# Kernel optimization log

Hardware: AMD Instinct MI355X
Metric: run time of the kernel (lower is better)

## Reference

```python
import jax, jax.numpy as jnp
import numpy as np

B, T, H, OUT = 16384, 128, 256, 10
EPS = 1e-5


def setup_inputs() -> dict:
    key = jax.random.key(0)
    ks = jax.random.split(key, 8)
    x = jax.random.randint(ks[0], (B, T, 1), 0, 10).astype(jnp.float32)
    def lin(k, fan_out, fan_in):
        bound = 1.0 / np.sqrt(fan_in)
        kw, kb = jax.random.split(k)
        w = jax.random.uniform(kw, (fan_out, fan_in), jnp.float32, -bound, bound)
        b = jax.random.uniform(kb, (fan_out,), jnp.float32, -bound, bound)
        return w, b
    embed_w, embed_b = lin(ks[1], H, 1)
    update_w, update_b = lin(ks[2], H, H)
    out_w, out_b = lin(ks[3], OUT, H)
    return {
        "x": x,
        "embed_w": embed_w, "embed_b": embed_b,
        "update_w": update_w, "update_b": update_b,
        "gamma": jnp.ones((H,), jnp.float32), "beta": jnp.zeros((H,), jnp.float32),
        "out_w": out_w, "out_b": out_b,
    }


def _layer_norm(h, gamma, beta):
    mu = jnp.mean(h, axis=-1, keepdims=True)
    var = jnp.mean(jnp.square(h - mu), axis=-1, keepdims=True)
    return (h - mu) * jax.lax.rsqrt(var + EPS) * gamma + beta


def reference(x, embed_w, embed_b, update_w, update_b, gamma, beta, out_w, out_b):
    # embed is per-timestep independent -> precompute for all T at once: [B,T,H]
    inp_all = jnp.tanh(jnp.einsum('bti,hi->bth', x, embed_w) + embed_b)

    def step(h, inp_t):  # h:[B,H], inp_t:[B,H]
        h = jnp.tanh((inp_t + h) @ update_w.T + update_b)
        h = _layer_norm(h, gamma, beta)
        return h, None

    h0 = jnp.zeros((x.shape[0], embed_w.shape[0]), x.dtype)
    h, _ = jax.lax.scan(step, h0, jnp.swapaxes(inp_all, 0, 1))  # scan over T
    return h @ out_w.T + out_b  # [B, 10]
```

## Files before the change

kernel.cpp:

```cpp
#include <hip/hip_runtime.h>
#include <hip/hip_fp16.h>
#include <math.h>

typedef _Float16 f16;
typedef _Float16 f16x8 __attribute__((ext_vector_type(8)));
typedef float f32x4 __attribute__((ext_vector_type(4)));
typedef unsigned char u8;

#define HDIM 256
#define TST 128
#define OUTD 10
#define S2LE 2.8853900817779268f

__global__ __launch_bounds__(256, 2) void rnn_kernel(
    const float* __restrict__ x,
    const float* __restrict__ embed_w,
    const float* __restrict__ embed_b,
    const float* __restrict__ update_w,
    const float* __restrict__ update_b,
    const float* __restrict__ gamma,
    const float* __restrict__ beta,
    const float* __restrict__ out_w,
    const float* __restrict__ out_b,
    float* __restrict__ out)
{
  __shared__ __align__(16) f16   sFR[2][2][8][64][8];
  __shared__ __align__(16) float sD1[10 * 260];
  __shared__ __align__(16) float sBW[HDIM];
  __shared__ __align__(16) float sRSg[HDIM];
  __shared__ __align__(16) float sST[2][32][12];
  __shared__ float sOB[16];
  __shared__ u8    sXb[TST][32];

  const int tid = threadIdx.x;
  const int w  = tid >> 6;
  const int l  = tid & 63;
  const int q  = l >> 4;
  const int ml = l & 15;
  const int base = blockIdx.x * 32;
  const int nb = w * 64 + q * 4;

  float* T0 = (float*)&sFR[0][0][0][0][0];

  {
    float ew = embed_w[tid], eb = embed_b[tid];
    #pragma unroll
    for (int xv = 0; xv < 10; xv++)
      T0[tid * 10 + xv] = tanhf((float)xv * ew + eb);
  }
  for (int idx = tid; idx < 32 * TST; idx += 256) {
    int col = idx >> 7, tt = idx & 127;
    sXb[tt][col] = (u8)(int)x[(size_t)(base + col) * TST + tt];
  }
  if (tid < 16) {
    float v = 0.f;
    if (tid < OUTD) {
      v = out_b[tid];
      const float* orow = out_w + tid * HDIM;
      for (int k = 0; k < HDIM; k += 4) {
        float4 wv = *(const float4*)(orow + k);
        float4 bv = *(const float4*)(beta + k);
        v = fmaf(wv.x, bv.x, fmaf(wv.y, bv.y, fmaf(wv.z, bv.z, fmaf(wv.w, bv.w, v))));
      }
    }
    sOB[tid] = v;
  }
  __syncthreads();

  {
    const int n = tid;
    const float* wrow = update_w + n * HDIM;
    float ty[10];
    #pragma unroll
    for (int xv = 0; xv < 10; xv++) ty[xv] = 0.f;
    float bw = 0.f, rsg = 0.f;
    for (int k = 0; k < HDIM; k += 4) {
      float4 wv4 = *(const float4*)(wrow + k);
      float4 b4  = *(const float4*)(beta + k);
      float4 g4  = *(const float4*)(gamma + k);
      bw  = fmaf(wv4.x, b4.x, fmaf(wv4.y, b4.y, fmaf(wv4.z, b4.z, fmaf(wv4.w, b4.w, bw))));
      rsg = fmaf(wv4.x, S2LE * g4.x, fmaf(wv4.y, S2LE * g4.y,
            fmaf(wv4.z, S2LE * g4.z, fmaf(wv4.w, S2LE * g4.w, rsg))));
      #pragma unroll
      for (int kk = 0; kk < 4; kk++) {
        float wv = ((const float*)&wv4)[kk];
        const float* t0r = T0 + (k + kk) * 10;
        #pragma unroll
        for (int xv = 0; xv < 10; xv++) ty[xv] = fmaf(wv, t0r[xv], ty[xv]);
      }
    }
    float ubn = update_b[n];
    sBW[n]  = S2LE * bw;
    sRSg[n] = rsg;
    #pragma unroll
    for (int xv = 0; xv < 10; xv++)
      sD1[xv * 260 + n] = S2LE * (ty[xv] + ubn + bw);
  }
  __syncthreads();

  f16x8 wf[4][8];
  #pragma unroll
  for (int c = 0; c < 8; c++) {
    const int k0 = c * 32 + q * 4;
    float4 g0 = *(const float4*)(gamma + k0);
    float4 g1 = *(const float4*)(gamma + k0 + 16);
    #pragma unroll
    for (int nt = 0; nt < 4; nt++) {
      const float* wrow = update_w + (w * 64 + nt * 16 + ml) * HDIM;
      float4 a0 = *(const float4*)(wrow + k0);
      float4 a1 = *(const float4*)(wrow + k0 + 16);
      f16x8 f;
      f[0]=(f16)(S2LE*g0.x*a0.x); f[1]=(f16)(S2LE*g0.y*a0.y);
      f[2]=(f16)(S2LE*g0.z*a0.z); f[3]=(f16)(S2LE*g0.w*a0.w);
      f[4]=(f16)(S2LE*g1.x*a1.x); f[5]=(f16)(S2LE*g1.y*a1.y);
      f[6]=(f16)(S2LE*g1.z*a1.z); f[7]=(f16)(S2LE*g1.w*a1.w);
      wf[nt][c] = f;
    }
  }
  f16x8 wf8[4];
  #pragma unroll
  for (int nt = 0; nt < 4; nt++) {
    const int n = w * 64 + nt * 16 + ml;
    f16x8 f;
    #pragma unroll
    for (int j = 0; j < 8; j++) {
      const int s = q * 4 + (j & 3) + 16 * (j >> 2);
      float v = (s < 10) ? sD1[s * 260 + n] : ((s == 10) ? sRSg[n] : 0.f);
      f[j] = (f16)v;
    }
    wf8[nt] = f;
  }

  f32x4 acc[2][4];
  {
    float p1g[2], p2g[2];
    #pragma unroll
    for (int g = 0; g < 2; g++) {
      const int xv0 = (int)sXb[0][g * 16 + ml];
      const float* dp = sD1 + xv0 * 260;
      float p1 = 0.f, p2 = 0.f;
      #pragma unroll
      for (int nt = 0; nt < 4; nt++) {
        f32x4 dd = *(const f32x4*)(dp + nb + nt * 16);
        f32x4 bw = *(const f32x4*)(sBW + nb + nt * 16);
        #pragma unroll
        for (int r = 0; r < 4; r++) {
          float y = dd[r] - bw[r];
          float e = __builtin_amdgcn_exp2f(y);
          float t = fmaf(-2.f, __builtin_amdgcn_rcpf(e + 1.f), 1.f);
          acc[g][nt][r] = t; p1 += t; p2 = fmaf(t, t, p2);
        }
      }
      p1g[g] = p1; p2g[g] = p2;
    }
    #pragma unroll
    for (int g = 0; g < 2; g++) {
      p1g[g] += __shfl_xor(p1g[g], 16, 64); p2g[g] += __shfl_xor(p2g[g], 16, 64);
      p1g[g] += __shfl_xor(p1g[g], 32, 64); p2g[g] += __shfl_xor(p2g[g], 32, 64);
    }
    #pragma unroll
    for (int g = 0; g < 2; g++) {
      #pragma unroll
      for (int cp = 0; cp < 2; cp++) {
        f16x8 af;
        #pragma unroll
        for (int j = 0; j < 8; j++) af[j] = (f16)acc[g][2 * cp + (j >> 2)][j & 3];
        *(f16x8*)&sFR[0][g][2 * w + cp][l][0] = af;
      }
    }
    if (l < 32) {
      int col = (l < 16) ? ml : (16 + ml);
      float2 v2 = (l < 16) ? make_float2(p1g[0], p2g[0]) : make_float2(p1g[1], p2g[1]);
      *(float2*)&sST[0][col][2 * w] = v2;
    }
    __syncthreads();
  }

  #pragma unroll 1
  for (int t = 1; t < TST; t++) {
    const int p = t & 1, pp = p ^ 1;
    const float* st0 = &sST[pp][ml][0];
    const float* st1 = &sST[pp][16 + ml][0];
    f32x4 u0 = *(const f32x4*)(st0);
    f32x4 u1 = *(const f32x4*)(st0 + 4);
    f32x4 v0 = *(const f32x4*)(st1);
    f32x4 v1 = *(const f32x4*)(st1 + 4);
    const int xva = (int)sXb[t][ml];
    const int xvb = (int)sXb[t][16 + ml];

    const f16* fb0 = &sFR[pp][0][0][0][0];
    const f16* fb1 = &sFR[pp][1][0][0][0];
    f16x8 rA0 = *(const f16x8*)(fb0 + l * 8);
    f16x8 rA1 = *(const f16x8*)(fb1 + l * 8);
    f16x8 rB0, rB1;

    #pragma unroll
    for (int g = 0; g < 2; g++)
      #pragma unroll
      for (int nt = 0; nt < 4; nt++)
        acc[g][nt] = (f32x4){0.f, 0.f, 0.f, 0.f};

    __builtin_amdgcn_s_setprio(1);
#define DO_C(CC, C0, C1, N0, N1)                                                  \
    {                                                                             \
      if ((CC) < 7) {                                                             \
        N0 = *(const f16x8*)(fb0 + ((CC) + 1) * 512 + l * 8);                     \
        N1 = *(const f16x8*)(fb1 + ((CC) + 1) * 512 + l * 8);                     \
      }                                                                           \
      acc[0][0] = __builtin_amdgcn_mfma_f32_16x16x32_f16(wf[0][CC], C0, acc[0][0],0,0,0); \
      acc[0][1] = __builtin_amdgcn_mfma_f32_16x16x32_f16(wf[1][CC], C0, acc[0][1],0,0,0); \
      acc[0][2] = __builtin_amdgcn_mfma_f32_16x16x32_f16(wf[2][CC], C0, acc[0][2],0,0,0); \
      acc[0][3] = __builtin_amdgcn_mfma_f32_16x16x32_f16(wf[3][CC], C0, acc[0][3],0,0,0); \
      acc[1][0] = __builtin_amdgcn_mfma_f32_16x16x32_f16(wf[0][CC], C1, acc[1][0],0,0,0); \
      acc[1][1] = __builtin_amdgcn_mfma_f32_16x16x32_f16(wf[1][CC], C1, acc[1][1],0,0,0); \
      acc[1][2] = __builtin_amdgcn_mfma_f32_16x16x32_f16(wf[2][CC], C1, acc[1][2],0,0,0); \
      acc[1][3] = __builtin_amdgcn_mfma_f32_16x16x32_f16(wf[3][CC], C1, acc[1][3],0,0,0); \
    }
    DO_C(0, rA0, rA1, rB0, rB1)
    DO_C(1, rB0, rB1, rA0, rA1)
    DO_C(2, rA0, rA1, rB0, rB1)
    DO_C(3, rB0, rB1, rA0, rA1)
    DO_C(4, rA0, rA1, rB0, rB1)
    DO_C(5, rB0, rB1, rA0, rA1)
    DO_C(6, rA0, rA1, rB0, rB1)
    DO_C(7, rB0, rB1, rA0, rA1)
#undef DO_C
    float s1a = (u0[0] + u0[2]) + (u1[0] + u1[2]);
    float s2a = (u0[1] + u0[3]) + (u1[1] + u1[3]);
    float s1b = (v0[0] + v0[2]) + (v1[0] + v1[2]);
    float s2b = (v0[1] + v0[3]) + (v1[1] + v1[3]);
    float mua = s1a * (1.f / 256.f);
    float vea = fmaf(s2a, 1.f / 256.f, -mua * mua) + 1e-5f;
    float rsa = __frsqrt_rn(vea);
    float iva = __builtin_amdgcn_sqrtf(vea);
    float mub = s1b * (1.f / 256.f);
    float veb = fmaf(s2b, 1.f / 256.f, -mub * mub) + 1e-5f;
    float rsb = __frsqrt_rn(veb);
    float ivb = __builtin_amdgcn_sqrtf(veb);
    f16x8 b8a, b8b;
    #pragma unroll
    for (int j = 0; j < 8; j++) {
      const int s = q * 4 + (j & 3) + 16 * (j >> 2);
      float va = (s == xva) ? iva : ((s == 10) ? -mua : 0.f);
      float vb = (s == xvb) ? ivb : ((s == 10) ? -mub : 0.f);
      b8a[j] = (f16)va; b8b[j] = (f16)vb;
    }
    acc[0][0] = __builtin_amdgcn_mfma_f32_16x16x32_f16(wf8[0], b8a, acc[0][0],0,0,0);
    acc[0][1] = __builtin_amdgcn_mfma_f32_16x16x32_f16(wf8[1], b8a, acc[0][1],0,0,0);
    acc[0][2] = __builtin_amdgcn_mfma_f32_16x16x32_f16(wf8[2], b8a, acc[0][2],0,0,0);
    acc[0][3] = __builtin_amdgcn_mfma_f32_16x16x32_f16(wf8[3], b8a, acc[0][3],0,0,0);
    acc[1][0] = __builtin_amdgcn_mfma_f32_16x16x32_f16(wf8[0], b8b, acc[1][0],0,0,0);
    acc[1][1] = __builtin_amdgcn_mfma_f32_16x16x32_f16(wf8[1], b8b, acc[1][1],0,0,0);
    acc[1][2] = __builtin_amdgcn_mfma_f32_16x16x32_f16(wf8[2], b8b, acc[1][2],0,0,0);
    acc[1][3] = __builtin_amdgcn_mfma_f32_16x16x32_f16(wf8[3], b8b, acc[1][3],0,0,0);
    __builtin_amdgcn_s_setprio(0);

    float p1g[2], p2g[2];
    #pragma unroll
    for (int g = 0; g < 2; g++) {
      const float rsg2 = (g == 0) ? rsa : rsb;
      float p1 = 0.f, p2 = 0.f;
      #pragma unroll
      for (int nt = 0; nt < 4; nt++) {
        #pragma unroll
        for (int r = 0; r < 4; r++) {
          float y = rsg2 * acc[g][nt][r];
          float e = __builtin_amdgcn_exp2f(y);
          float tv = fmaf(-2.f, __builtin_amdgcn_rcpf(e + 1.f), 1.f);
          acc[g][nt][r] = tv; p1 += tv; p2 = fmaf(tv, tv, p2);
        }
      }
      p1g[g] = p1; p2g[g] = p2;
    }
    #pragma unroll
    for (int g = 0; g < 2; g++) {
      #pragma unroll
      for (int cp = 0; cp < 2; cp++) {
        f16x8 af;
        #pragma unroll
        for (int j = 0; j < 8; j++) af[j] = (f16)acc[g][2 * cp + (j >> 2)][j & 3];
        *(f16x8*)&sFR[p][g][2 * w + cp][l][0] = af;
      }
    }
    #pragma unroll
    for (int g = 0; g < 2; g++) {
      p1g[g] += __shfl_xor(p1g[g], 16, 64); p2g[g] += __shfl_xor(p2g[g], 16, 64);
      p1g[g] += __shfl_xor(p1g[g], 32, 64); p2g[g] += __shfl_xor(p2g[g], 32, 64);
    }
    if (l < 32) {
      int col = (l < 16) ? ml : (16 + ml);
      float2 v2 = (l < 16) ? make_float2(p1g[0], p2g[0]) : make_float2(p1g[1], p2g[1]);
      *(float2*)&sST[p][col][2 * w] = v2;
    }
    __syncthreads();
  }

  {
    const float* st0 = &sST[1][ml][0];
    const float* st1 = &sST[1][16 + ml][0];
    f32x4 u0 = *(const f32x4*)(st0);
    f32x4 u1 = *(const f32x4*)(st0 + 4);
    f32x4 v0 = *(const f32x4*)(st1);
    f32x4 v1 = *(const f32x4*)(st1 + 4);
    float s1a = (u0[0] + u0[2]) + (u1[0] + u1[2]);
    float s2a = (u0[1] + u0[3]) + (u1[1] + u1[3]);
    float s1b = (v0[0] + v0[2]) + (v1[0] + v1[2]);
    float s2b = (v0[1] + v0[3]) + (v1[1] + v1[3]);
    float rs_f[2], nrsmu[2];
    {
      float mua = s1a * (1.f / 256.f);
      float vea = fmaf(s2a, 1.f / 256.f, -mua * mua) + 1e-5f;
      rs_f[0] = __frsqrt_rn(vea); nrsmu[0] = -rs_f[0] * mua;
      float mub = s1b * (1.f / 256.f);
      float veb = fmaf(s2b, 1.f / 256.f, -mub * mub) + 1e-5f;
      rs_f[1] = __frsqrt_rn(veb); nrsmu[1] = -rs_f[1] * mub;
    }
    f16* sOW = (f16*)sD1;
    for (int idx = tid; idx < 512; idx += 256) {
      int c = idx >> 6, l2 = idx & 63, q2 = l2 >> 4, o = l2 & 15;
      int k0 = c * 32 + q2 * 4;
      f16x8 f;
      #pragma unroll
      for (int j = 0; j < 8; j++) f[j] = (f16)0.f;
      if (o < OUTD) {
        const float* orow = out_w + o * HDIM;
        float4 a0 = *(const float4*)(orow + k0);
        float4 a1 = *(const float4*)(orow + k0 + 16);
        float4 g0 = *(const float4*)(gamma + k0);
        float4 g1 = *(const float4*)(gamma + k0 + 16);
        f[0]=(f16)(g0.x*a0.x); f[1]=(f16)(g0.y*a0.y); f[2]=(f16)(g0.z*a0.z); f[3]=(f16)(g0.w*a0.w);
        f[4]=(f16)(g1.x*a1.x); f[5]=(f16)(g1.y*a1.y); f[6]=(f16)(g1.z*a1.z); f[7]=(f16)(g1.w*a1.w);
      }
      *(f16x8*)(sOW + idx * 8) = f;
    }
    __syncthreads();
    float* sOut = (float*)&sFR[1][0][0][0][0];
    #pragma unroll
    for (int g = 0; g < 2; g++) {
      f32x4 aO = {0.f, 0.f, 0.f, 0.f};
      #pragma unroll
      for (int cp = 0; cp < 2; cp++) {
        f16x8 af;
        #pragma unroll
        for (int j = 0; j < 8; j++)
          af[j] = (f16)fmaf(rs_f[g], acc[g][2 * cp + (j >> 2)][j & 3], nrsmu[g]);
        f16x8 of = *(const f16x8*)(sOW + ((size_t)(2 * w + cp) * 64 + l) * 8);
        aO = __builtin_amdgcn_mfma_f32_16x16x32_f16(of, af, aO, 0, 0, 0);
      }
      #pragma unroll
      for (int r = 0; r < 4; r++)
        sOut[((g * 4 + w) * 16 + ml) * 16 + q * 4 + r] = aO[r];
    }
    __syncthreads();
    for (int idx = tid; idx < 32 * OUTD; idx += 256) {
      int m = idx / OUTD, o = idx - m * OUTD;
      int g = m >> 4, mm = m & 15;
      float s = 0.f;
      #pragma unroll
      for (int ww = 0; ww < 4; ww++) s += sOut[((g * 4 + ww) * 16 + mm) * 16 + o];
      out[(size_t)(base + m) * OUTD + o] = s + sOB[o];
    }
  }
}

extern "C" void kernel_launch(void* const* d_in, const int* in_sizes, int n_in,
                              void* d_out, int out_size, void* d_ws, size_t ws_size,
                              hipStream_t stream) {
  const float* x   = (const float*)d_in[0];
  const float* ew  = (const float*)d_in[1];
  const float* eb  = (const float*)d_in[2];
  const float* uw  = (const float*)d_in[3];
  const float* ub  = (const float*)d_in[4];
  const float* g   = (const float*)d_in[5];
  const float* be  = (const float*)d_in[6];
  const float* ow  = (const float*)d_in[7];
  const float* ob  = (const float*)d_in[8];
  float* out = (float*)d_out;

  const int B = in_sizes[0] / TST;
  const int grid = B / 32;
  hipLaunchKernelGGL(rnn_kernel, dim3(grid), dim3(256), 0, stream,
                     x, ew, eb, uw, ub, g, be, ow, ob, out);
}
```

Baseline: 375.3 us.

## Replace correction MFMA with per-element FMA epilogue and unroll timesteps by two

Removes the extra per-step MFMA that folded the embedding term and layernorm mean correction into the accumulator. These terms are now applied in the tanh epilogue as fmas using an fp32 embedding row and a gamma-scaled row-sum vector kept in registers. It also converts activations with packed round-toward-zero fp16 conversions and unrolls the time loop by two so the ping-pong buffer indices become compile-time constants. The final projection reads the last hidden state from shared memory instead of registers. The trade is extra loads of embedding rows and more VALU work per element against one fewer MFMA pass per step, plus slightly different rounding.

```diff
diff --git a/kernel.cpp b/kernel.cpp
--- a/kernel.cpp
+++ b/kernel.cpp
@@ -3,6 +3,7 @@
 #include <math.h>
 
 typedef _Float16 f16;
+typedef _Float16 f16x2 __attribute__((ext_vector_type(2)));
 typedef _Float16 f16x8 __attribute__((ext_vector_type(8)));
 typedef float f32x4 __attribute__((ext_vector_type(4)));
 typedef unsigned char u8;
@@ -11,6 +12,11 @@
 #define TST 128
 #define OUTD 10
 #define S2LE 2.8853900817779268f
+
+static __device__ __forceinline__ f16x2 pkrtz(float a, float b) {
+  auto r = __builtin_amdgcn_cvt_pkrtz(a, b);
+  return *(f16x2*)&r;
+}
 
 __global__ __launch_bounds__(256, 2) void rnn_kernel(
     const float* __restrict__ x,
@@ -117,183 +123,164 @@
       wf[nt][c] = f;
     }
   }
-  f16x8 wf8[4];
+  f32x4 rsgr[4];
   #pragma unroll
-  for (int nt = 0; nt < 4; nt++) {
-    const int n = w * 64 + nt * 16 + ml;
-    f16x8 f;
-    #pragma unroll
-    for (int j = 0; j < 8; j++) {
-      const int s = q * 4 + (j & 3) + 16 * (j >> 2);
-      float v = (s < 10) ? sD1[s * 260 + n] : ((s == 10) ? sRSg[n] : 0.f);
-      f[j] = (f16)v;
-    }
-    wf8[nt] = f;
-  }
-
-  f32x4 acc[2][4];
+  for (int nt = 0; nt < 4; nt++)
+    rsgr[nt] = *(const f32x4*)(sRSg + nb + nt * 16);
+
   {
-    float p1g[2], p2g[2];
+    float p1g_[2], p2g_[2];
     #pragma unroll
     for (int g = 0; g < 2; g++) {
       const int xv0 = (int)sXb[0][g * 16 + ml];
       const float* dp = sD1 + xv0 * 260;
       float p1 = 0.f, p2 = 0.f;
       #pragma unroll
-      for (int nt = 0; nt < 4; nt++) {
-        f32x4 dd = *(const f32x4*)(dp + nb + nt * 16);
-        f32x4 bw = *(const f32x4*)(sBW + nb + nt * 16);
+      for (int cp = 0; cp < 2; cp++) {
+        union { f16x8 v8; f16x2 v2[4]; } pk;
         #pragma unroll
-        for (int r = 0; r < 4; r++) {
-          float y = dd[r] - bw[r];
-          float e = __builtin_amdgcn_exp2f(y);
-          float t = fmaf(-2.f, __builtin_amdgcn_rcpf(e + 1.f), 1.f);
-          acc[g][nt][r] = t; p1 += t; p2 = fmaf(t, t, p2);
+        for (int h = 0; h < 2; h++) {
+          const int nt = 2 * cp + h;
+          f32x4 dd = *(const f32x4*)(dp + nb + nt * 16);
+          f32x4 bw = *(const f32x4*)(sBW + nb + nt * 16);
+          float tq[4];
+          #pragma unroll
+          for (int r = 0; r < 4; r++) {
+            float y = dd[r] - bw[r];
+            float e = __builtin_amdgcn_exp2f(y);
+            float tv = fmaf(-2.f, __builtin_amdgcn_rcpf(e + 1.f), 1.f);
+            tq[r] = tv; p1 += tv; p2 = fmaf(tv, tv, p2);
+          }
+          pk.v2[2 * h]     = pkrtz(tq[0], tq[1]);
+          pk.v2[2 * h + 1] = pkrtz(tq[2], tq[3]);
         }
-      }
-      p1g[g] = p1; p2g[g] = p2;
+        *(f16x8*)&sFR[0][g][2 * w + cp][l][0] = pk.v8;
+      }
+      p1g_[g] = p1; p2g_[g] = p2;
     }
     #pragma unroll
     for (int g = 0; g < 2; g++) {
-      p1g[g] += __shfl_xor(p1g[g], 16, 64); p2g[g] += __shfl_xor(p2g[g], 16, 64);
-      p1g[g] += __shfl_xor(p1g[g], 32, 64); p2g[g] += __shfl_xor(p2g[g], 32, 64);
-    }
-    #pragma unroll
-    for (int g = 0; g < 2; g++) {
-      #pragma unroll
-      for (int cp = 0; cp < 2; cp++) {
-        f16x8 af;
-        #pragma unroll
-        for (int j = 0; j < 8; j++) af[j] = (f16)acc[g][2 * cp + (j >> 2)][j & 3];
-        *(f16x8*)&sFR[0][g][2 * w + cp][l][0] = af;
-      }
+      p1g_[g] += __shfl_xor(p1g_[g], 16, 64); p2g_[g] += __shfl_xor(p2g_[g], 16, 64);
+      p1g_[g] += __shfl_xor(p1g_[g], 32, 64); p2g_[g] += __shfl_xor(p2g_[g], 32, 64);
     }
     if (l < 32) {
       int col = (l < 16) ? ml : (16 + ml);
-      float2 v2 = (l < 16) ? make_float2(p1g[0], p2g[0]) : make_float2(p1g[1], p2g[1]);
+      float2 v2 = (l < 16) ? make_float2(p1g_[0], p2g_[0]) : make_float2(p1g_[1], p2g_[1]);
       *(float2*)&sST[0][col][2 * w] = v2;
     }
     __syncthreads();
   }
 
+#define MM8(CC, C0, C1, N0, N1)                                                \
+    {                                                                          \
+      if ((CC) < 7) {                                                          \
+        N0 = *(const f16x8*)(fb0_ + ((CC) + 1) * 512 + l * 8);                 \
+        N1 = *(const f16x8*)(fb1_ + ((CC) + 1) * 512 + l * 8);                 \
+      }                                                                        \
+      acc_[0][0] = __builtin_amdgcn_mfma_f32_16x16x32_f16(wf[0][CC], C0, acc_[0][0],0,0,0); \
+      acc_[0][1] = __builtin_amdgcn_mfma_f32_16x16x32_f16(wf[1][CC], C0, acc_[0][1],0,0,0); \
+      acc_[0][2] = __builtin_amdgcn_mfma_f32_16x16x32_f16(wf[2][CC], C0, acc_[0][2],0,0,0); \
+      acc_[0][3] = __builtin_amdgcn_mfma_f32_16x16x32_f16(wf[3][CC], C0, acc_[0][3],0,0,0); \
+      acc_[1][0] = __builtin_amdgcn_mfma_f32_16x16x32_f16(wf[0][CC], C1, acc_[1][0],0,0,0); \
+      acc_[1][1] = __builtin_amdgcn_mfma_f32_16x16x32_f16(wf[1][CC], C1, acc_[1][1],0,0,0); \
+      acc_[1][2] = __builtin_amdgcn_mfma_f32_16x16x32_f16(wf[2][CC], C1, acc_[1][2],0,0,0); \
+      acc_[1][3] = __builtin_amdgcn_mfma_f32_16x16x32_f16(wf[3][CC], C1, acc_[1][3],0,0,0); \
+    }
+
+#define STEP(T, P, PP)                                                         \
+  {                                                                            \
+    const float* st0_ = &sST[PP][ml][0];                                       \
+    const float* st1_ = &sST[PP][16 + ml][0];                                  \
+    f32x4 u0_ = *(const f32x4*)(st0_);                                         \
+    f32x4 u1_ = *(const f32x4*)(st0_ + 4);                                     \
+    f32x4 v0_ = *(const f32x4*)(st1_);                                         \
+    f32x4 v1_ = *(const f32x4*)(st1_ + 4);                                     \
+    const int xva_ = (int)sXb[T][ml];                                          \
+    const int xvb_ = (int)sXb[T][16 + ml];                                     \
+    const f16* fb0_ = &sFR[PP][0][0][0][0];                                    \
+    const f16* fb1_ = &sFR[PP][1][0][0][0];                                    \
+    const float* dpa_ = sD1 + xva_ * 260 + nb;                                 \
+    const float* dpb_ = sD1 + xvb_ * 260 + nb;                                 \
+    f32x4 dda_[4], ddb_[4];                                                    \
+    _Pragma("unroll") for (int n_ = 0; n_ < 4; n_++) {                         \
+      dda_[n_] = *(const f32x4*)(dpa_ + n_ * 16);                              \
+      ddb_[n_] = *(const f32x4*)(dpb_ + n_ * 16);                              \
+    }                                                                          \
+    f16x8 rA0_ = *(const f16x8*)(fb0_ + l * 8);                                \
+    f16x8 rA1_ = *(const f16x8*)(fb1_ + l * 8);                                \
+    f16x8 rB0_, rB1_;                                                          \
+    f32x4 acc_[2][4];                                                          \
+    _Pragma("unroll") for (int g_ = 0; g_ < 2; g_++)                           \
+      _Pragma("unroll") for (int n_ = 0; n_ < 4; n_++)                         \
+        acc_[g_][n_] = (f32x4){0.f, 0.f, 0.f, 0.f};                            \
+    __builtin_amdgcn_s_setprio(1);                                             \
+    MM8(0, rA0_, rA1_, rB0_, rB1_)                                             \
+    MM8(1, rB0_, rB1_, rA0_, rA1_)                                             \
+    MM8(2, rA0_, rA1_, rB0_, rB1_)                                             \
+    MM8(3, rB0_, rB1_, rA0_, rA1_)                                             \
+    MM8(4, rA0_, rA1_, rB0_, rB1_)                                             \
+    MM8(5, rB0_, rB1_, rA0_, rA1_)                                             \
+    MM8(6, rA0_, rA1_, rB0_, rB1_)                                             \
+    MM8(7, rB0_, rB1_, rA0_, rA1_)                                             \
+    __builtin_amdgcn_s_setprio(0);                                             \
+    float s1a_ = (u0_[0] + u0_[2]) + (u1_[0] + u1_[2]);                        \
+    float s2a_ = (u0_[1] + u0_[3]) + (u1_[1] + u1_[3]);                        \
+    float s1b_ = (v0_[0] + v0_[2]) + (v1_[0] + v1_[2]);                        \
+    float s2b_ = (v0_[1] + v0_[3]) + (v1_[1] + v1_[3]);                        \
+    float mua_ = s1a_ * (1.f / 256.f);                                         \
+    float rsa_ = __frsqrt_rn(fmaf(s2a_, 1.f / 256.f, -mua_ * mua_) + 1e-5f);   \
+    float mub_ = s1b_ * (1.f / 256.f);                                         \
+    float rsb_ = __frsqrt_rn(fmaf(s2b_, 1.f / 256.f, -mub_ * mub_) + 1e-5f);   \
+    float rma_ = rsa_ * mua_;                                                  \
+    float rmb_ = rsb_ * mub_;                                                  \
+    float p1a_ = 0.f, p2a_ = 0.f, p1b_ = 0.f, p2b_ = 0.f;                      \
+    _Pragma("unroll") for (int cp_ = 0; cp_ < 2; cp_++) {                      \
+      union { f16x8 v8; f16x2 v2[4]; } ka_, kb_;                               \
+      _Pragma("unroll") for (int h_ = 0; h_ < 2; h_++) {                       \
+        const int nt_ = 2 * cp_ + h_;                                          \
+        float ta_[4], tb_[4];                                                  \
+        _Pragma("unroll") for (int r_ = 0; r_ < 4; r_++) {                     \
+          float ya_ = fmaf(rsa_, acc_[0][nt_][r_],                             \
+                       fmaf(-rma_, rsgr[nt_][r_], dda_[nt_][r_]));             \
+          float ea_ = __builtin_amdgcn_exp2f(ya_);                             \
+          float va_ = fmaf(-2.f, __builtin_amdgcn_rcpf(ea_ + 1.f), 1.f);       \
+          ta_[r_] = va_; p1a_ += va_; p2a_ = fmaf(va_, va_, p2a_);             \
+          float yb_ = fmaf(rsb_, acc_[1][nt_][r_],                             \
+                       fmaf(-rmb_, rsgr[nt_][r_], ddb_[nt_][r_]));             \
+          float eb_ = __builtin_amdgcn_exp2f(yb_);                             \
+          float vb_ = fmaf(-2.f, __builtin_amdgcn_rcpf(eb_ + 1.f), 1.f);       \
+          tb_[r_] = vb_; p1b_ += vb_; p2b_ = fmaf(vb_, vb_, p2b_);             \
+        }                                                                      \
+        ka_.v2[2 * h_]     = pkrtz(ta_[0], ta_[1]);                            \
+        ka_.v2[2 * h_ + 1] = pkrtz(ta_[2], ta_[3]);                            \
+        kb_.v2[2 * h_]     = pkrtz(tb_[0], tb_[1]);                            \
+        kb_.v2[2 * h_ + 1] = pkrtz(tb_[2], tb_[3]);                            \
+      }                                                                        \
+      *(f16x8*)&sFR[P][0][2 * w + cp_][l][0] = ka_.v8;                         \
+      *(f16x8*)&sFR[P][1][2 * w + cp_][l][0] = kb_.v8;                         \
+    }                                                                          \
+    p1a_ += __shfl_xor(p1a_, 16, 64); p2a_ += __shfl_xor(p2a_, 16, 64);        \
+    p1a_ += __shfl_xor(p1a_, 32, 64); p2a_ += __shfl_xor(p2a_, 32, 64);        \
+    p1b_ += __shfl_xor(p1b_, 16, 64); p2b_ += __shfl_xor(p2b_, 16, 64);        \
+    p1b_ += __shfl_xor(p1b_, 32, 64); p2b_ += __shfl_xor(p2b_, 32, 64);        \
+    if (l < 32) {                                                              \
+      int col_ = (l < 16) ? ml : (16 + ml);                                    \
+      float2 w2_ = (l < 16) ? make_float2(p1a_, p2a_)                          \
+                            : make_float2(p1b_, p2b_);                         \
+      *(float2*)&sST[P][col_][2 * w] = w2_;                                    \
+    }                                                                          \
+    __syncthreads();                                                           \
+  }
+
   #pragma unroll 1
-  for (int t = 1; t < TST; t++) {
-    const int p = t & 1, pp = p ^ 1;
-    const float* st0 = &sST[pp][ml][0];
-    const float* st1 = &sST[pp][16 + ml][0];
-    f32x4 u0 = *(const f32x4*)(st0);
-    f32x4 u1 = *(const f32x4*)(st0 + 4);
-    f32x4 v0 = *(const f32x4*)(st1);
-    f32x4 v1 = *(const f32x4*)(st1 + 4);
-    const int xva = (int)sXb[t][ml];
-    const int xvb = (int)sXb[t][16 + ml];
-
-    const f16* fb0 = &sFR[pp][0][0][0][0];
-    const f16* fb1 = &sFR[pp][1][0][0][0];
-    f16x8 rA0 = *(const f16x8*)(fb0 + l * 8);
-    f16x8 rA1 = *(const f16x8*)(fb1 + l * 8);
-    f16x8 rB0, rB1;
-
-    #pragma unroll
-    for (int g = 0; g < 2; g++)
-      #pragma unroll
-      for (int nt = 0; nt < 4; nt++)
-        acc[g][nt] = (f32x4){0.f, 0.f, 0.f, 0.f};
-
-    __builtin_amdgcn_s_setprio(1);
-#define DO_C(CC, C0, C1, N0, N1)                                                  \
-    {                                                                             \
-      if ((CC) < 7) {                                                             \
-        N0 = *(const f16x8*)(fb0 + ((CC) + 1) * 512 + l * 8);                     \
-        N1 = *(const f16x8*)(fb1 + ((CC) + 1) * 512 + l * 8);                     \
-      }                                                                           \
-      acc[0][0] = __builtin_amdgcn_mfma_f32_16x16x32_f16(wf[0][CC], C0, acc[0][0],0,0,0); \
-      acc[0][1] = __builtin_amdgcn_mfma_f32_16x16x32_f16(wf[1][CC], C0, acc[0][1],0,0,0); \
-      acc[0][2] = __builtin_amdgcn_mfma_f32_16x16x32_f16(wf[2][CC], C0, acc[0][2],0,0,0); \
-      acc[0][3] = __builtin_amdgcn_mfma_f32_16x16x32_f16(wf[3][CC], C0, acc[0][3],0,0,0); \
-      acc[1][0] = __builtin_amdgcn_mfma_f32_16x16x32_f16(wf[0][CC], C1, acc[1][0],0,0,0); \
-      acc[1][1] = __builtin_amdgcn_mfma_f32_16x16x32_f16(wf[1][CC], C1, acc[1][1],0,0,0); \
-      acc[1][2] = __builtin_amdgcn_mfma_f32_16x16x32_f16(wf[2][CC], C1, acc[1][2],0,0,0); \
-      acc[1][3] = __builtin_amdgcn_mfma_f32_16x16x32_f16(wf[3][CC], C1, acc[1][3],0,0,0); \
-    }
-    DO_C(0, rA0, rA1, rB0, rB1)
-    DO_C(1, rB0, rB1, rA0, rA1)
-    DO_C(2, rA0, rA1, rB0, rB1)
-    DO_C(3, rB0, rB1, rA0, rA1)
-    DO_C(4, rA0, rA1, rB0, rB1)
-    DO_C(5, rB0, rB1, rA0, rA1)
-    DO_C(6, rA0, rA1, rB0, rB1)
-    DO_C(7, rB0, rB1, rA0, rA1)
-#undef DO_C
-    float s1a = (u0[0] + u0[2]) + (u1[0] + u1[2]);
-    float s2a = (u0[1] + u0[3]) + (u1[1] + u1[3]);
-    float s1b = (v0[0] + v0[2]) + (v1[0] + v1[2]);
-    float s2b = (v0[1] + v0[3]) + (v1[1] + v1[3]);
-    float mua = s1a * (1.f / 256.f);
-    float vea = fmaf(s2a, 1.f / 256.f, -mua * mua) + 1e-5f;
-    float rsa = __frsqrt_rn(vea);
-    float iva = __builtin_amdgcn_sqrtf(vea);
-    float mub = s1b * (1.f / 256.f);
-    float veb = fmaf(s2b, 1.f / 256.f, -mub * mub) + 1e-5f;
-    float rsb = __frsqrt_rn(veb);
-    float ivb = __builtin_amdgcn_sqrtf(veb);
-    f16x8 b8a, b8b;
-    #pragma unroll
-    for (int j = 0; j < 8; j++) {
-      const int s = q * 4 + (j & 3) + 16 * (j >> 2);
-      float va = (s == xva) ? iva : ((s == 10) ? -mua : 0.f);
-      float vb = (s == xvb) ? ivb : ((s == 10) ? -mub : 0.f);
-      b8a[j] = (f16)va; b8b[j] = (f16)vb;
-    }
-    acc[0][0] = __builtin_amdgcn_mfma_f32_16x16x32_f16(wf8[0], b8a, acc[0][0],0,0,0);
-    acc[0][1] = __builtin_amdgcn_mfma_f32_16x16x32_f16(wf8[1], b8a, acc[0][1],0,0,0);
-    acc[0][2] = __builtin_amdgcn_mfma_f32_16x16x32_f16(wf8[2], b8a, acc[0][2],0,0,0);
-    acc[0][3] = __builtin_amdgcn_mfma_f32_16x16x32_f16(wf8[3], b8a, acc[0][3],0,0,0);
-    acc[1][0] = __builtin_amdgcn_mfma_f32_16x16x32_f16(wf8[0], b8b, acc[1][0],0,0,0);
-    acc[1][1] = __builtin_amdgcn_mfma_f32_16x16x32_f16(wf8[1], b8b, acc[1][1],0,0,0);
-    acc[1][2] = __builtin_amdgcn_mfma_f32_16x16x32_f16(wf8[2], b8b, acc[1][2],0,0,0);
-    acc[1][3] = __builtin_amdgcn_mfma_f32_16x16x32_f16(wf8[3], b8b, acc[1][3],0,0,0);
-    __builtin_amdgcn_s_setprio(0);
-
-    float p1g[2], p2g[2];
-    #pragma unroll
-    for (int g = 0; g < 2; g++) {
-      const float rsg2 = (g == 0) ? rsa : rsb;
-      float p1 = 0.f, p2 = 0.f;
-      #pragma unroll
-      for (int nt = 0; nt < 4; nt++) {
-        #pragma unroll
-        for (int r = 0; r < 4; r++) {
-          float y = rsg2 * acc[g][nt][r];
-          float e = __builtin_amdgcn_exp2f(y);
-          float tv = fmaf(-2.f, __builtin_amdgcn_rcpf(e + 1.f), 1.f);
-          acc[g][nt][r] = tv; p1 += tv; p2 = fmaf(tv, tv, p2);
-        }
-      }
-      p1g[g] = p1; p2g[g] = p2;
-    }
-    #pragma unroll
-    for (int g = 0; g < 2; g++) {
-      #pragma unroll
-      for (int cp = 0; cp < 2; cp++) {
-        f16x8 af;
-        #pragma unroll
-        for (int j = 0; j < 8; j++) af[j] = (f16)acc[g][2 * cp + (j >> 2)][j & 3];
-        *(f16x8*)&sFR[p][g][2 * w + cp][l][0] = af;
-      }
-    }
-    #pragma unroll
-    for (int g = 0; g < 2; g++) {
-      p1g[g] += __shfl_xor(p1g[g], 16, 64); p2g[g] += __shfl_xor(p2g[g], 16, 64);
-      p1g[g] += __shfl_xor(p1g[g], 32, 64); p2g[g] += __shfl_xor(p2g[g], 32, 64);
-    }
-    if (l < 32) {
-      int col = (l < 16) ? ml : (16 + ml);
-      float2 v2 = (l < 16) ? make_float2(p1g[0], p2g[0]) : make_float2(p1g[1], p2g[1]);
-      *(float2*)&sST[p][col][2 * w] = v2;
-    }
-    __syncthreads();
-  }
+  for (int tt = 1; tt <= 125; tt += 2) {
+    STEP(tt, 1, 0)
+    STEP(tt + 1, 0, 1)
+  }
+  STEP(127, 1, 0)
+
+#undef STEP
+#undef MM8
 
   {
     const float* st0 = &sST[1][ml][0];
@@ -334,16 +321,17 @@
       *(f16x8*)(sOW + idx * 8) = f;
     }
     __syncthreads();
-    float* sOut = (float*)&sFR[1][0][0][0][0];
+    float* sOut = (float*)&sFR[0][0][0][0][0];
     #pragma unroll
     for (int g = 0; g < 2; g++) {
       f32x4 aO = {0.f, 0.f, 0.f, 0.f};
       #pragma unroll
       for (int cp = 0; cp < 2; cp++) {
+        f16x8 fr = *(const f16x8*)&sFR[1][g][2 * w + cp][l][0];
         f16x8 af;
         #pragma unroll
         for (int j = 0; j < 8; j++)
-          af[j] = (f16)fmaf(rs_f[g], acc[g][2 * cp + (j >> 2)][j & 3], nrsmu[g]);
+          af[j] = (f16)fmaf(rs_f[g], (float)fr[j], nrsmu[g]);
         f16x8 of = *(const f16x8*)(sOW + ((size_t)(2 * w + cp) * 64 + l) * 8);
         aO = __builtin_amdgcn_mfma_f32_16x16x32_f16(of, af, aO, 0, 0, 0);
       }
```

Result: slower. 385.8 us (+2.8%).
